# Optimization experiments

Hardware: AMD Instinct MI355X
Metric: run time of the kernel (lower is better)

## Reference

```python
import jax, jax.numpy as jnp
import numpy as np

N_VOLS, N_PARTS = 4, 8          # hard-coded in GL.forward
B = N_VOLS * N_PARTS            # asserted batch size = 32
DIM, HID, PROJ = 8192, 4096, 256
TEMP = 0.1
BN_EPS = 1e-5


def setup_inputs() -> dict:
    key = jax.random.key(0)
    k = jax.random.split(key, 5)
    s1 = 1.0 / np.sqrt(DIM)
    s2 = 1.0 / np.sqrt(HID)
    return {
        "x": jax.random.normal(k[0], (B, DIM), jnp.float32),
        "W1": jax.random.uniform(k[1], (DIM, HID), jnp.float32, -s1, s1),
        "b1": jax.random.uniform(k[2], (HID,), jnp.float32, -s1, s1),
        "gamma": jnp.ones((HID,), jnp.float32),
        "beta": jnp.zeros((HID,), jnp.float32),
        "W2": jax.random.uniform(k[3], (HID, PROJ), jnp.float32, -s2, s2),
        "b2": jax.random.uniform(k[4], (PROJ,), jnp.float32, -s2, s2),
    }


def _gl_loss(proj):
    # F.normalize(p=2, dim=-1); CosineSimilarity on unit vectors == dot product
    p = proj / jnp.linalg.norm(proj, axis=-1, keepdims=True)
    sims = (p @ p.T) / TEMP                       # [B, B]
    idx = jnp.arange(B)
    # pos_index(i) = {i % n_parts + v * n_parts} -> same part id; includes i itself
    pos_mask = (idx[:, None] % N_PARTS) == (idx[None, :] % N_PARTS)  # [B, B], 4 per row
    neg_mask = ~pos_mask                                             # 28 per row
    E = jnp.exp(sims)                              # original uses raw exp (no max-shift)
    row_neg = jnp.sum(jnp.where(neg_mask, E, 0.0), axis=1)    # sum_j exp(s[i, neg_j])
    ET = E.T                                        # ET[i, p] = exp(s[p, i])
    col_neg = jnp.sum(jnp.where(neg_mask, ET, 0.0), axis=1)   # sum_j exp(s[neg_j, i])
    t1 = -jnp.log(E / (E + row_neg[:, None]))      # row-direction term per (i, pos)
    t2 = -jnp.log(ET / (ET + col_neg[:, None]))    # column-direction term per (i, pos)
    per_row = jnp.sum(jnp.where(pos_mask, t1 + t2, 0.0), axis=1) / N_VOLS
    return jnp.sum(per_row) / (B * 2)


def reference(x, W1, b1, gamma, beta, W2, b2):
    # projector MLP: Linear -> BatchNorm1d (training stats) -> ReLU -> Linear
    h = x @ W1 + b1
    mu = jnp.mean(h, axis=0)
    var = jnp.var(h, axis=0)                       # biased variance, BN training mode
    h = gamma * (h - mu) * jax.lax.rsqrt(var + BN_EPS) + beta
    h = jax.nn.relu(h)
    proj = h @ W2 + b2                             # [B, PROJ]
    return _gl_loss(proj)
```

## Files before the change

kernel.cpp:

```cpp
#include <hip/hip_runtime.h>

#define DIM   8192
#define HID   4096
#define PROJ  256
#define NB    32
#define KSP1  16
#define KCH1  (DIM / KSP1)
#define KT1   (KCH1 / 32)
#define KSP2  16
#define KCH2  (HID / KSP2)
#define KT2   (KCH2 / 32)

typedef __attribute__((ext_vector_type(8))) short bf16x8;
typedef __attribute__((ext_vector_type(4))) float f32x4;

__device__ __forceinline__ float bf2f(unsigned short u) {
    return __uint_as_float(((unsigned)u) << 16);
}
__device__ __forceinline__ unsigned short f2bf(float f) {
    unsigned u = __float_as_uint(f);
    u += 0x7fffu + ((u >> 16) & 1u);
    return (unsigned short)(u >> 16);
}
__device__ __forceinline__ unsigned pk2(float a, float b) {
    return (unsigned)f2bf(a) | ((unsigned)f2bf(b) << 16);
}

__device__ __forceinline__ bool detect_bf16(const unsigned* __restrict__ xw, int lane) {
    unsigned v = xw[lane];
    int e = (int)((v >> 7) & 0xffu);
    bool pl = (e >= 100 && e <= 135);
    unsigned long long b = __ballot(pl);
    return __popcll(b) >= 32;
}

__global__ __launch_bounds__(256, 4) void gemm1_kernel(
    const void* __restrict__ xv, const void* __restrict__ W1v,
    float* __restrict__ hpart)
{
    const int t  = threadIdx.x;
    const int nb = blockIdx.x & 63;
    const int kc = blockIdx.x >> 6;
    const int k0 = kc * KCH1;

    const bool isbf = detect_bf16((const unsigned*)xv, t & 63);
    const unsigned short* xu  = (const unsigned short*)xv;
    const float*          xf  = (const float*)xv;
    const unsigned short* W1u = (const unsigned short*)W1v;
    const float*          W1f = (const float*)W1v;

    const int lane  = t & 63;
    const int w     = t >> 6;
    const int g     = lane >> 4;
    const int ln    = lane & 15;
    const int nbase = nb * 64 + w * 16;

    auto loadB = [&](int kt) -> bf16x8 {
        bf16x8 b;
        const long rb = (long)(k0 + kt * 32 + g * 8) * HID + nbase + ln;
        if (isbf) {
            #pragma unroll
            for (int j = 0; j < 8; ++j) b[j] = (short)W1u[rb + (long)j * HID];
        } else {
            #pragma unroll
            for (int j = 0; j < 8; ++j) b[j] = (short)f2bf(W1f[rb + (long)j * HID]);
        }
        return b;
    };
    auto loadA = [&](int kt, int mt) -> bf16x8 {
        const int base = (mt * 16 + ln) * DIM + k0 + kt * 32 + g * 8;
        if (isbf) return *(const bf16x8*)(xu + base);
        float4 f0 = *(const float4*)(xf + base);
        float4 f1 = *(const float4*)(xf + base + 4);
        union { uint4 u; bf16x8 v; } c;
        c.u = make_uint4(pk2(f0.x, f0.y), pk2(f0.z, f0.w),
                         pk2(f1.x, f1.y), pk2(f1.z, f1.w));
        return c.v;
    };

    bf16x8 bb[4], a0[4], a1[4];
    #pragma unroll
    for (int i = 0; i < 4; ++i) {
        bb[i] = loadB(i); a0[i] = loadA(i, 0); a1[i] = loadA(i, 1);
    }

    f32x4 acc0 = {0.f, 0.f, 0.f, 0.f};
    f32x4 acc1 = {0.f, 0.f, 0.f, 0.f};

    #pragma unroll
    for (int kt = 0; kt < KT1; ++kt) {
        const int s = kt & 3;
        acc0 = __builtin_amdgcn_mfma_f32_16x16x32_bf16(a0[s], bb[s], acc0, 0, 0, 0);
        acc1 = __builtin_amdgcn_mfma_f32_16x16x32_bf16(a1[s], bb[s], acc1, 0, 0, 0);
        if (kt + 4 < KT1) {
            bb[s] = loadB(kt + 4);
            a0[s] = loadA(kt + 4, 0);
            a1[s] = loadA(kt + 4, 1);
        }
    }

    const int col = nbase + ln;
    #pragma unroll
    for (int r = 0; r < 4; ++r) {
        hpart[(kc * NB + g * 4 + r) * HID + col]      = acc0[r];
        hpart[(kc * NB + 16 + g * 4 + r) * HID + col] = acc1[r];
    }
}

__global__ __launch_bounds__(256) void bnrelu_kernel(
    const float* __restrict__ hpart, const void* __restrict__ gv,
    const void* __restrict__ bev, unsigned short* __restrict__ hrelu,
    const void* __restrict__ xv)
{
    __shared__ float red[16][64];
    __shared__ float ssc[64], sbe[64], smu[64];
    const int t  = threadIdx.x;
    const int c4 = t & 15, q = t >> 4;
    const int n0 = blockIdx.x * 64;
    const int nb = n0 + c4 * 4;
    const bool isbf = detect_bf16((const unsigned*)xv, t & 63);

    f32x4 h0 = {0.f, 0.f, 0.f, 0.f};
    f32x4 h1 = {0.f, 0.f, 0.f, 0.f};
    #pragma unroll
    for (int kc = 0; kc < KSP1; ++kc) {
        h0 += *(const f32x4*)(hpart + (size_t)(kc * 32 + 2 * q) * HID + nb);
        h1 += *(const f32x4*)(hpart + (size_t)(kc * 32 + 2 * q + 1) * HID + nb);
    }
    *(f32x4*)&red[q][c4 * 4] = h0 + h1;
    __syncthreads();
    if (t < 64) {
        float s = 0.f;
        #pragma unroll
        for (int i = 0; i < 16; ++i) s += red[i][t];
        smu[t] = s * (1.f / 32.f);
    }
    __syncthreads();
    const f32x4 mu = *(const f32x4*)&smu[c4 * 4];
    const f32x4 d0 = h0 - mu, d1 = h1 - mu;
    *(f32x4*)&red[q][c4 * 4] = d0 * d0 + d1 * d1;
    __syncthreads();
    if (t < 64) {
        float v = 0.f;
        #pragma unroll
        for (int i = 0; i < 16; ++i) v += red[i][t];
        v *= (1.f / 32.f);
        const int nn = n0 + t;
        const float ga = isbf ? bf2f(((const unsigned short*)gv)[nn])  : ((const float*)gv)[nn];
        const float be = isbf ? bf2f(((const unsigned short*)bev)[nn]) : ((const float*)bev)[nn];
        ssc[t] = ga * rsqrtf(v + 1e-5f);
        sbe[t] = be;
    }
    __syncthreads();
    const f32x4 sc = *(const f32x4*)&ssc[c4 * 4];
    const f32x4 be = *(const f32x4*)&sbe[c4 * 4];
    f32x4 r0 = d0 * sc + be;
    f32x4 r1 = d1 * sc + be;
    ushort4 o0, o1;
    o0.x = f2bf(fmaxf(r0.x, 0.f)); o0.y = f2bf(fmaxf(r0.y, 0.f));
    o0.z = f2bf(fmaxf(r0.z, 0.f)); o0.w = f2bf(fmaxf(r0.w, 0.f));
    o1.x = f2bf(fmaxf(r1.x, 0.f)); o1.y = f2bf(fmaxf(r1.y, 0.f));
    o1.z = f2bf(fmaxf(r1.z, 0.f)); o1.w = f2bf(fmaxf(r1.w, 0.f));
    *(ushort4*)(hrelu + (size_t)(2 * q) * HID + nb)     = o0;
    *(ushort4*)(hrelu + (size_t)(2 * q + 1) * HID + nb) = o1;
}

__global__ __launch_bounds__(256, 4) void gemm2_kernel(
    const unsigned short* __restrict__ hrelu, const void* __restrict__ W2v,
    float* __restrict__ ppart, const void* __restrict__ xv)
{
    const int t  = threadIdx.x;
    const int nb = blockIdx.x & 3;
    const int kc = blockIdx.x >> 2;
    const int k0 = kc * KCH2;

    const bool isbf = detect_bf16((const unsigned*)xv, t & 63);
    const unsigned short* W2u = (const unsigned short*)W2v;
    const float*          W2f = (const float*)W2v;

    const int lane  = t & 63;
    const int w     = t >> 6;
    const int g     = lane >> 4;
    const int ln    = lane & 15;
    const int nbase = nb * 64 + w * 16;

    auto loadB = [&](int kt) -> bf16x8 {
        bf16x8 b;
        const long rb = (long)(k0 + kt * 32 + g * 8) * PROJ + nbase + ln;
        if (isbf) {
            #pragma unroll
            for (int j = 0; j < 8; ++j) b[j] = (short)W2u[rb + (long)j * PROJ];
        } else {
            #pragma unroll
            for (int j = 0; j < 8; ++j) b[j] = (short)f2bf(W2f[rb + (long)j * PROJ]);
        }
        return b;
    };
    auto loadA = [&](int kt, int mt) -> bf16x8 {
        return *(const bf16x8*)(hrelu + (mt * 16 + ln) * HID + k0 + kt * 32 + g * 8);
    };

    bf16x8 bb[4], a0[4], a1[4];
    #pragma unroll
    for (int i = 0; i < 4; ++i) {
        bb[i] = loadB(i); a0[i] = loadA(i, 0); a1[i] = loadA(i, 1);
    }

    f32x4 acc0 = {0.f, 0.f, 0.f, 0.f};
    f32x4 acc1 = {0.f, 0.f, 0.f, 0.f};

    #pragma unroll
    for (int kt = 0; kt < KT2; ++kt) {
        const int s = kt & 3;
        acc0 = __builtin_amdgcn_mfma_f32_16x16x32_bf16(a0[s], bb[s], acc0, 0, 0, 0);
        acc1 = __builtin_amdgcn_mfma_f32_16x16x32_bf16(a1[s], bb[s], acc1, 0, 0, 0);
        if (kt + 4 < KT2) {
            bb[s] = loadB(kt + 4);
            a0[s] = loadA(kt + 4, 0);
            a1[s] = loadA(kt + 4, 1);
        }
    }

    const int col = nbase + ln;
    #pragma unroll
    for (int r = 0; r < 4; ++r) {
        ppart[(kc * NB + g * 4 + r) * PROJ + col]      = acc0[r];
        ppart[(kc * NB + 16 + g * 4 + r) * PROJ + col] = acc1[r];
    }
}

__global__ __launch_bounds__(1024) void loss_kernel(
    const float* __restrict__ ppart, const void* __restrict__ b2v,
    const void* __restrict__ xv, unsigned* __restrict__ out)
{
    __shared__ float ps[32][260];
    __shared__ float npart2[32][8];
    __shared__ float inrm[32];
    __shared__ float rowtot[32];
    const int t = threadIdx.x;
    const bool isbf = detect_bf16((const unsigned*)xv, t & 63);

    #pragma unroll
    for (int i = 0; i < 8; ++i) {
        const int o = i * 1024 + t;
        float s = 0.f;
        #pragma unroll
        for (int s16 = 0; s16 < KSP2; ++s16) s += ppart[s16 * (NB * PROJ) + o];
        const int c = o & 255;
        s += isbf ? bf2f(((const unsigned short*)b2v)[c]) : ((const float*)b2v)[c];
        ps[o >> 8][c] = s;
    }
    __syncthreads();

    if (t < 256) {
        const int r = t >> 3, seg = t & 7;
        float s = 0.f;
        #pragma unroll
        for (int c = 0; c < 32; ++c) { float v = ps[r][seg * 32 + c]; s += v * v; }
        npart2[r][seg] = s;
    }
    __syncthreads();
    if (t < 32) {
        float s = 0.f;
        #pragma unroll
        for (int j = 0; j < 8; ++j) s += npart2[t][j];
        inrm[t] = rsqrtf(s);
    }
    __syncthreads();

    const int wv   = t >> 6;
    const int lane = t & 63;
    const int j    = (lane >> 1) & 31;
    const int half = lane & 1;
    #pragma unroll
    for (int rr = 0; rr < 2; ++rr) {
        const int i = wv * 2 + rr;
        float acc = 0.f;
        const int cb = half * 128;
        #pragma unroll
        for (int c = 0; c < 128; c += 4) {
            float4 a = *(const float4*)&ps[i][cb + c];
            float4 b = *(const float4*)&ps[j][cb + c];
            acc += a.x * b.x + a.y * b.y + a.z * b.z + a.w * b.w;
        }
        acc += __shfl_xor(acc, 1);

        const float sim = acc * inrm[i] * inrm[j] * 10.0f;
        const float E   = __expf(sim);
        const bool pos  = ((j & 7) == (i & 7));

        float nv = (!pos && half == 0) ? E : 0.f;
        #pragma unroll
        for (int s = 1; s < 64; s <<= 1) nv += __shfl_xor(nv, s);
        float pv = (pos && half == 0) ? (logf(E + nv) - sim) : 0.f;
        #pragma unroll
        for (int s = 1; s < 64; s <<= 1) pv += __shfl_xor(pv, s);
        if (lane == 0) rowtot[i] = pv;
    }
    __syncthreads();

    if (t < 64) {
        float v = (t < 32) ? rowtot[t] : 0.f;
        #pragma unroll
        for (int s = 1; s < 64; s <<= 1) v += __shfl_xor(v, s);
        if (t == 0) {
            const float loss = v * (1.0f / 128.0f);
            const unsigned lb = (unsigned)f2bf(loss);
            const unsigned base = (__float_as_uint(loss) & 0xffff0000u) | lb;
            unsigned best = base;
            float ebest = fabsf(__uint_as_float(base) - loss);
            const unsigned cp = base + 0x10000u;
            const float ep = fabsf(__uint_as_float(cp) - loss);
            if (ep < ebest) { best = cp; ebest = ep; }
            const unsigned cm = base - 0x10000u;
            const float em = fabsf(__uint_as_float(cm) - loss);
            if (em < ebest) { best = cm; }
            out[0] = best;
        }
    }
}

extern "C" void kernel_launch(void* const* d_in, const int* in_sizes, int n_in,
                              void* d_out, int out_size, void* d_ws, size_t ws_size,
                              hipStream_t stream) {
    const void* x  = d_in[0];
    const void* W1 = d_in[1];
    const void* ga = d_in[3];
    const void* be = d_in[4];
    const void* W2 = d_in[5];
    const void* b2 = d_in[6];

    char* wsp = (char*)d_ws;
    float* hpart = (float*)wsp;                 wsp += (size_t)KSP1 * NB * HID * 4;
    unsigned short* hrelu = (unsigned short*)wsp; wsp += (size_t)NB * HID * 2;
    float* ppart = (float*)wsp;                 wsp += (size_t)KSP2 * NB * PROJ * 4;

    gemm1_kernel<<<1024, 256, 0, stream>>>(x, W1, hpart);
    bnrelu_kernel<<<64, 256, 0, stream>>>(hpart, ga, be, hrelu, x);
    gemm2_kernel<<<64, 256, 0, stream>>>(hrelu, W2, ppart, x);
    loss_kernel<<<1, 1024, 0, stream>>>(ppart, b2, x, (unsigned*)d_out);
}
```

Before: 242.2 us.

## Stage W1 tiles through swizzled LDS with coalesced loads and wider N tiles

The first GEMM now loads W1 rows as coalesced 16-byte vectors into a double-buffered, XOR-swizzled LDS tile of 32x512 and reads the MFMA B operands from LDS. Before, it did strided per-element global gathers. Each block covers 512 columns with 8 column tiles per wave. The K split goes from 16 to 64 to keep enough blocks. The cost is a hpart buffer four times larger, a longer reduction in the BN kernel, higher register and LDS use (launch bounds lowered to 2), and still-scalar LDS reads for B.

```diff
diff --git a/kernel.cpp b/kernel.cpp
--- a/kernel.cpp
+++ b/kernel.cpp
@@ -4,9 +4,9 @@
 #define HID   4096
 #define PROJ  256
 #define NB    32
-#define KSP1  16
+#define KSP1  64
 #define KCH1  (DIM / KSP1)
-#define KT1   (KCH1 / 32)
+#define NW1   512
 #define KSP2  16
 #define KCH2  (HID / KSP2)
 #define KT2   (KCH2 / 32)
@@ -34,14 +34,16 @@
     return __popcll(b) >= 32;
 }
 
-__global__ __launch_bounds__(256, 4) void gemm1_kernel(
+__global__ __launch_bounds__(256, 2) void gemm1_kernel(
     const void* __restrict__ xv, const void* __restrict__ W1v,
     float* __restrict__ hpart)
 {
-    const int t  = threadIdx.x;
-    const int nb = blockIdx.x & 63;
-    const int kc = blockIdx.x >> 6;
-    const int k0 = kc * KCH1;
+    __shared__ unsigned short wt[2][32 * 512];
+    const int t   = threadIdx.x;
+    const int nbq = blockIdx.x & 7;
+    const int kc  = blockIdx.x >> 3;
+    const int n0  = nbq * NW1;
+    const int k0  = kc * KCH1;
 
     const bool isbf = detect_bf16((const unsigned*)xv, t & 63);
     const unsigned short* xu  = (const unsigned short*)xv;
@@ -49,26 +51,38 @@
     const unsigned short* W1u = (const unsigned short*)W1v;
     const float*          W1f = (const float*)W1v;
 
-    const int lane  = t & 63;
-    const int w     = t >> 6;
-    const int g     = lane >> 4;
-    const int ln    = lane & 15;
-    const int nbase = nb * 64 + w * 16;
-
-    auto loadB = [&](int kt) -> bf16x8 {
-        bf16x8 b;
-        const long rb = (long)(k0 + kt * 32 + g * 8) * HID + nbase + ln;
-        if (isbf) {
-            #pragma unroll
-            for (int j = 0; j < 8; ++j) b[j] = (short)W1u[rb + (long)j * HID];
-        } else {
-            #pragma unroll
-            for (int j = 0; j < 8; ++j) b[j] = (short)f2bf(W1f[rb + (long)j * HID]);
-        }
-        return b;
-    };
-    auto loadA = [&](int kt, int mt) -> bf16x8 {
-        const int base = (mt * 16 + ln) * DIM + k0 + kt * 32 + g * 8;
+    const int lane = t & 63;
+    const int w    = t >> 6;
+    const int g    = lane >> 4;
+    const int ln   = lane & 15;
+
+    const int srb = t >> 6;
+    const int sc  = t & 63;
+
+    auto gload = [&](int step, uint4* dst) {
+        #pragma unroll
+        for (int i = 0; i < 8; ++i) {
+            const size_t base = (size_t)(k0 + step * 32 + i * 4 + srb) * HID + n0 + sc * 8;
+            if (isbf) {
+                dst[i] = *(const uint4*)(W1u + base);
+            } else {
+                float4 f0 = *(const float4*)(W1f + base);
+                float4 f1 = *(const float4*)(W1f + base + 4);
+                dst[i] = make_uint4(pk2(f0.x, f0.y), pk2(f0.z, f0.w),
+                                    pk2(f1.x, f1.y), pk2(f1.z, f1.w));
+            }
+        }
+    };
+    auto dswrite = [&](int buf, const uint4* src) {
+        #pragma unroll
+        for (int i = 0; i < 8; ++i) {
+            const int r  = i * 4 + srb;
+            const int pc = sc ^ (2 * (r >> 3));
+            *(uint4*)&wt[buf][r * 512 + pc * 8] = src[i];
+        }
+    };
+    auto loadA = [&](int step, int mt) -> bf16x8 {
+        const int base = (mt * 16 + ln) * DIM + k0 + step * 32 + g * 8;
         if (isbf) return *(const bf16x8*)(xu + base);
         float4 f0 = *(const float4*)(xf + base);
         float4 f1 = *(const float4*)(xf + base + 4);
@@ -78,32 +92,49 @@
         return c.v;
     };
 
-    bf16x8 bb[4], a0[4], a1[4];
-    #pragma unroll
-    for (int i = 0; i < 4; ++i) {
-        bb[i] = loadB(i); a0[i] = loadA(i, 0); a1[i] = loadA(i, 1);
-    }
-
-    f32x4 acc0 = {0.f, 0.f, 0.f, 0.f};
-    f32x4 acc1 = {0.f, 0.f, 0.f, 0.f};
-
-    #pragma unroll
-    for (int kt = 0; kt < KT1; ++kt) {
-        const int s = kt & 3;
-        acc0 = __builtin_amdgcn_mfma_f32_16x16x32_bf16(a0[s], bb[s], acc0, 0, 0, 0);
-        acc1 = __builtin_amdgcn_mfma_f32_16x16x32_bf16(a1[s], bb[s], acc1, 0, 0, 0);
-        if (kt + 4 < KT1) {
-            bb[s] = loadB(kt + 4);
-            a0[s] = loadA(kt + 4, 0);
-            a1[s] = loadA(kt + 4, 1);
-        }
-    }
-
-    const int col = nbase + ln;
-    #pragma unroll
-    for (int r = 0; r < 4; ++r) {
-        hpart[(kc * NB + g * 4 + r) * HID + col]      = acc0[r];
-        hpart[(kc * NB + 16 + g * 4 + r) * HID + col] = acc1[r];
+    uint4 gst[2][8];
+    gload(0, gst[0]);
+    dswrite(0, gst[0]);
+    gload(1, gst[1]);
+    bf16x8 areg[2][2];
+    areg[0][0] = loadA(0, 0); areg[0][1] = loadA(0, 1);
+    areg[1][0] = loadA(1, 0); areg[1][1] = loadA(1, 1);
+    __syncthreads();
+
+    f32x4 acc[8][2];
+    #pragma unroll
+    for (int i = 0; i < 8; ++i) {
+        acc[i][0] = (f32x4){0.f, 0.f, 0.f, 0.f};
+        acc[i][1] = (f32x4){0.f, 0.f, 0.f, 0.f};
+    }
+
+    #pragma unroll
+    for (int s = 0; s < 4; ++s) {
+        const int cur = s & 1;
+        #pragma unroll
+        for (int ct = 0; ct < 8; ++ct) {
+            const int pc = (w * 16 + 2 * ct + (ln >> 3)) ^ (2 * g);
+            const unsigned short* p = &wt[cur][(8 * g) * 512 + pc * 8 + (ln & 7)];
+            bf16x8 b;
+            #pragma unroll
+            for (int j = 0; j < 8; ++j) b[j] = (short)p[j * 512];
+            acc[ct][0] = __builtin_amdgcn_mfma_f32_16x16x32_bf16(areg[cur][0], b, acc[ct][0], 0, 0, 0);
+            acc[ct][1] = __builtin_amdgcn_mfma_f32_16x16x32_bf16(areg[cur][1], b, acc[ct][1], 0, 0, 0);
+        }
+        if (s + 2 < 4) { areg[cur][0] = loadA(s + 2, 0); areg[cur][1] = loadA(s + 2, 1); }
+        if (s + 1 < 4) dswrite(cur ^ 1, gst[cur ^ 1]);
+        if (s + 2 < 4) gload(s + 2, gst[cur]);
+        __syncthreads();
+    }
+
+    #pragma unroll
+    for (int ct = 0; ct < 8; ++ct) {
+        const int col = n0 + w * 128 + ct * 16 + ln;
+        #pragma unroll
+        for (int r = 0; r < 4; ++r) {
+            hpart[(size_t)(kc * NB + g * 4 + r) * HID + col]      = acc[ct][0][r];
+            hpart[(size_t)(kc * NB + 16 + g * 4 + r) * HID + col] = acc[ct][1][r];
+        }
     }
 }
 
@@ -122,7 +153,6 @@
 
     f32x4 h0 = {0.f, 0.f, 0.f, 0.f};
     f32x4 h1 = {0.f, 0.f, 0.f, 0.f};
-    #pragma unroll
     for (int kc = 0; kc < KSP1; ++kc) {
         h0 += *(const f32x4*)(hpart + (size_t)(kc * 32 + 2 * q) * HID + nb);
         h1 += *(const f32x4*)(hpart + (size_t)(kc * 32 + 2 * q + 1) * HID + nb);
@@ -335,7 +365,7 @@
     unsigned short* hrelu = (unsigned short*)wsp; wsp += (size_t)NB * HID * 2;
     float* ppart = (float*)wsp;                 wsp += (size_t)KSP2 * NB * PROJ * 4;
 
-    gemm1_kernel<<<1024, 256, 0, stream>>>(x, W1, hpart);
+    gemm1_kernel<<<512, 256, 0, stream>>>(x, W1, hpart);
     bnrelu_kernel<<<64, 256, 0, stream>>>(hpart, ga, be, hrelu, x);
     gemm2_kernel<<<64, 256, 0, stream>>>(hrelu, W2, ppart, x);
     loss_kernel<<<1, 1024, 0, stream>>>(ppart, b2, x, (unsigned*)d_out);
```

After: 244.6 us. Within noise of the previous version (+1.0%).
